# Kernel tuning notes

Hardware: AMD Instinct MI355X
Metric: run time of the kernel (lower is better)

The kernel has to match this reference:

```python
import jax, jax.numpy as jnp
import numpy as np

B, S, H, D = 8, 1024, 16, 64
EMBED_DIM = H * D  # 1024
NEG_INF = -1e30


def setup_inputs() -> dict:
    key = jax.random.key(0)
    kq, kk, kv, kl = jax.random.split(key, 4)
    q = jax.random.normal(kq, (B, S, H, D), dtype=jnp.float32)
    k = jax.random.normal(kk, (B, S, H, D), dtype=jnp.float32)
    v = jax.random.normal(kv, (B, S, H, D), dtype=jnp.float32)
    # ragged lengths in [S//4, S]; prefix-style key_padding_mask (True = valid)
    lengths = jax.random.randint(kl, (B,), S // 4, S + 1)
    key_padding_mask = jnp.arange(S)[None, :] < lengths[:, None]
    return {"q": q, "k": k, "v": v, "key_padding_mask": key_padding_mask}


def reference(q, k, v, key_padding_mask):
    # Equivalent math of flash_attn_unpadded_qkvpacked_func on unpadded tokens
    # followed by pad_input (zeros at padded query rows), dropout=0 (eval).
    # NOTE: module uses softmax_scale = embed_dim ** -0.5 (not head_dim).
    scale = EMBED_DIM ** (-0.5)
    scores = jnp.einsum("bqhd,bkhd->bhqk", q, k) * scale  # [B,H,S,S]
    scores = jnp.where(key_padding_mask[:, None, None, :], scores, NEG_INF)
    attn = jax.nn.softmax(scores, axis=-1)
    out = jnp.einsum("bhqk,bkhd->bqhd", attn, v)  # [B,S,H,D]
    # pad_input re-inserts zeros at padded query positions
    out = out * key_padding_mask[:, :, None, None].astype(out.dtype)
    return out.reshape(B, S, H * D)
```

## Files before the change

kernel.cpp:

```cpp
#include <hip/hip_runtime.h>


#define SS 1024
#define NH 16
#define DD 64
#define ROWSTRIDE (NH * DD)
#define SCALE 0.03125f
#define LOG2E 1.4426950408889634f
#define PC1 (SCALE * LOG2E)
#define PC2 (-12.0f * LOG2E)
#define KSTR 72
#define VSTR 72

typedef short bf16x8 __attribute__((ext_vector_type(8)));
typedef unsigned short u16;
typedef unsigned short u16x8 __attribute__((ext_vector_type(8)));
typedef unsigned short u16x4 __attribute__((ext_vector_type(4)));
typedef float f32x4 __attribute__((ext_vector_type(4)));
typedef unsigned u32x4 __attribute__((ext_vector_type(4)));

__device__ __forceinline__ u16 f2bf(float x) {
  unsigned u = __builtin_bit_cast(unsigned, x);
  return (u16)((u + 0x7FFFu + ((u >> 16) & 1u)) >> 16);
}
__device__ __forceinline__ float bf2f(u16 s) {
  unsigned u = ((unsigned)s) << 16;
  return __builtin_bit_cast(float, u);
}
__device__ __forceinline__ unsigned pkbf(float a, float b) {
#if __has_builtin(__builtin_amdgcn_cvt_pk_bf16_f32)
  auto r = __builtin_amdgcn_cvt_pk_bf16_f32(a, b);
  return __builtin_bit_cast(unsigned, r);
#else
  return (unsigned)f2bf(a) | ((unsigned)f2bf(b) << 16);
#endif
}

__global__ __launch_bounds__(256, 4) void fa_main(const void* qv, const void* kv,
                                                  const void* vv, const void* maskv,
                                                  float* out) {
  __shared__ __attribute__((aligned(16))) u16 Kt[64 * KSTR];
  __shared__ __attribute__((aligned(16))) u16 Vt[64 * VSTR + 64];

  int tid = threadIdx.x;
  int lane = tid & 63;
  int w = tid >> 6;
  int t = lane & 15;
  int quad = lane >> 4;

  int bid = blockIdx.x;
  int x = bid & 7;
  int j = bid >> 3;
  int qt = j & 15;
  int bh = ((j >> 4) << 3) + x;
  int h = bh & (NH - 1);
  int b = bh >> 4;
  int q0 = qt * 64;

  const u16* qs16 = (const u16*)qv;
  float dv = bf2f(qs16[2 * lane]);
  unsigned long long bal = __ballot(!(fabsf(dv) < 100.0f));
  int isf32 = (__popcll(bal) >= 16) ? 1 : 0;

  const unsigned char* m8 = (const unsigned char*)maskv;
  const int* m32 = (const int*)maskv;
  bool isu8 = (m8[1] != 0);
  int lo = 0, hi = SS;
  while (lo < hi) {
    int mid = (lo + hi) >> 1;
    int vbit = isu8 ? (m8[b * SS + mid] != 0) : (m32[b * SS + mid] != 0);
    if (vbit) lo = mid + 1; else hi = mid;
  }
  int len = lo;

  size_t base = (size_t)b * SS * ROWSTRIDE + h * DD;

  if (q0 >= len) {
    f32x4 z4 = {0.f, 0.f, 0.f, 0.f};
    for (int i = tid; i < 64 * 16; i += 256) {
      int r = i >> 4, dseg = (i & 15) << 2;
      *(f32x4*)&out[base + (size_t)(q0 + r) * ROWSTRIDE + dseg] = z4;
    }
    return;
  }

  int qrow = q0 + w * 16 + t;
  bf16x8 qf[2];
  if (isf32) {
    const float* qp = (const float*)qv + base + (size_t)qrow * ROWSTRIDE + quad * 8;
#pragma unroll
    for (int kk = 0; kk < 2; kk++) {
      union { bf16x8 v; unsigned d[4]; } u;
#pragma unroll
      for (int jj = 0; jj < 4; jj++)
        u.d[jj] = pkbf(qp[kk * 32 + 2 * jj], qp[kk * 32 + 2 * jj + 1]);
      qf[kk] = u.v;
    }
  } else {
    const u16* qp = (const u16*)qv + base + (size_t)qrow * ROWSTRIDE + quad * 8;
#pragma unroll
    for (int kk = 0; kk < 2; kk++) qf[kk] = *(const bf16x8*)(qp + kk * 32);
  }

  f32x4 zero4 = {0.f, 0.f, 0.f, 0.f};
  f32x4 oacc[4];
#pragma unroll
  for (int c = 0; c < 4; c++) oacc[c] = zero4;
  float lsum = 0.f;

  int key = tid >> 2, seg = tid & 3;
  int kp = tid >> 3, ds = tid & 7;
  int nkt = (len + 63) >> 6;

  f32x4 kA[4], vA[4];
  u16x8 kB[2], vB[2];

  auto issue_loads = [&](int kt) {
    int krow = kt * 64 + key;
    if (krow > SS - 1) krow = SS - 1;
    int vrow = kt * 64 + 2 * kp;
    if (vrow > SS - 2) vrow = SS - 2;
    size_t ksrc = base + (size_t)krow * ROWSTRIDE + seg * 16;
    size_t vsrc = base + (size_t)vrow * ROWSTRIDE + ds * 8;
    if (isf32) {
      const f32x4* kpp = (const f32x4*)((const float*)kv + ksrc);
#pragma unroll
      for (int i = 0; i < 4; i++) kA[i] = kpp[i];
      const float* vp = (const float*)vv + vsrc;
      vA[0] = *(const f32x4*)vp;
      vA[1] = *(const f32x4*)(vp + 4);
      vA[2] = *(const f32x4*)(vp + ROWSTRIDE);
      vA[3] = *(const f32x4*)(vp + ROWSTRIDE + 4);
    } else {
      const u16x8* kpp = (const u16x8*)((const u16*)kv + ksrc);
      kB[0] = kpp[0]; kB[1] = kpp[1];
      const u16* vp = (const u16*)vv + vsrc;
      vB[0] = *(const u16x8*)vp;
      vB[1] = *(const u16x8*)(vp + ROWSTRIDE);
    }
  };

  auto stage_to_lds = [&]() {
    if (isf32) {
      unsigned kd[8];
#pragma unroll
      for (int i = 0; i < 8; i++)
        kd[i] = pkbf(kA[i >> 1][2 * (i & 1)], kA[i >> 1][2 * (i & 1) + 1]);
      *(u32x4*)&Kt[key * KSTR + seg * 16] = u32x4{kd[0], kd[1], kd[2], kd[3]};
      *(u32x4*)&Kt[key * KSTR + seg * 16 + 8] = u32x4{kd[4], kd[5], kd[6], kd[7]};
#pragma unroll
      for (int jj = 0; jj < 8; jj++) {
        int d = ds * 8 + jj;
        *(unsigned*)&Vt[d * VSTR + (d >> 4) * 16 + 2 * kp] =
            pkbf(vA[jj >> 2][jj & 3], vA[2 + (jj >> 2)][jj & 3]);
      }
    } else {
      *(u16x8*)&Kt[key * KSTR + seg * 16] = kB[0];
      *(u16x8*)&Kt[key * KSTR + seg * 16 + 8] = kB[1];
#pragma unroll
      for (int jj = 0; jj < 8; jj++) {
        int d = ds * 8 + jj;
        *(unsigned*)&Vt[d * VSTR + (d >> 4) * 16 + 2 * kp] =
            (unsigned)(u16)vB[0][jj] | ((unsigned)(u16)vB[1][jj] << 16);
      }
    }
  };

  issue_loads(0);

  for (int kt = 0; kt < nkt; ++kt) {
    __syncthreads();
    stage_to_lds();
    if (kt + 1 < nkt) issue_loads(kt + 1);
    __syncthreads();

    f32x4 sacc[4];
#pragma unroll
    for (int c = 0; c < 4; c++) sacc[c] = zero4;
#pragma unroll
    for (int kk = 0; kk < 2; kk++) {
#pragma unroll
      for (int c = 0; c < 4; c++) {
        bf16x8 ka = *(const bf16x8*)&Kt[(c * 16 + t) * KSTR + kk * 32 + quad * 8];
        sacc[c] = __builtin_amdgcn_mfma_f32_16x16x32_bf16(ka, qf[kk], sacc[c], 0, 0, 0);
      }
    }

    float p[4][4];
    if (kt == nkt - 1) {
      int krem = len - kt * 64;
#pragma unroll
      for (int c = 0; c < 4; c++) {
        int kbase = c * 16 + quad * 4;
#pragma unroll
        for (int r = 0; r < 4; r++)
          p[c][r] = (kbase + r < krem)
                        ? __builtin_amdgcn_exp2f(fmaf(sacc[c][r], PC1, PC2))
                        : 0.0f;
      }
    } else {
#pragma unroll
      for (int c = 0; c < 4; c++)
#pragma unroll
        for (int r = 0; r < 4; r++)
          p[c][r] = __builtin_amdgcn_exp2f(fmaf(sacc[c][r], PC1, PC2));
    }
#pragma unroll
    for (int c = 0; c < 4; c++)
      lsum += (p[c][0] + p[c][1]) + (p[c][2] + p[c][3]);

    unsigned pd[4][2];
#pragma unroll
    for (int c = 0; c < 4; c++) {
      pd[c][0] = pkbf(p[c][0], p[c][1]);
      pd[c][1] = pkbf(p[c][2], p[c][3]);
    }

#pragma unroll
    for (int kc = 0; kc < 2; kc++) {
      union { bf16x8 v; unsigned d[4]; } pa;
      pa.d[0] = pd[2 * kc][0];
      pa.d[1] = pd[2 * kc][1];
      pa.d[2] = pd[2 * kc + 1][0];
      pa.d[3] = pd[2 * kc + 1][1];
#pragma unroll
      for (int c = 0; c < 4; c++) {
        const u16* vr = &Vt[(c * 16 + t) * VSTR + c * 16 + kc * 32 + quad * 4];
        union { bf16x8 v; u16x4 h[2]; } vb;
        vb.h[0] = *(const u16x4*)vr;
        vb.h[1] = *(const u16x4*)(vr + 16);
        oacc[c] = __builtin_amdgcn_mfma_f32_16x16x32_bf16(pa.v, vb.v, oacc[c], 0, 0, 0);
      }
    }
  }

  lsum += __shfl_xor(lsum, 16);
  lsum += __shfl_xor(lsum, 32);
  float inv[4];
#pragma unroll
  for (int r = 0; r < 4; r++)
    inv[r] = 1.0f / __shfl(lsum, quad * 4 + r);
#pragma unroll
  for (int c = 0; c < 4; c++)
#pragma unroll
    for (int r = 0; r < 4; r++) {
      int qr = q0 + w * 16 + quad * 4 + r;
      float o = oacc[c][r] * inv[r];
      out[base + (size_t)qr * ROWSTRIDE + c * 16 + t] = (qr < len) ? o : 0.0f;
    }
}

extern "C" void kernel_launch(void* const* d_in, const int* in_sizes, int n_in,
                              void* d_out, int out_size, void* d_ws, size_t ws_size,
                              hipStream_t stream) {
  fa_main<<<2048, 256, 0, stream>>>(d_in[0], d_in[1], d_in[2], d_in[3], (float*)d_out);
}
```

Measured before the change: 173.9 us.

## Use persistent workers with atomic work queue for attention tiles

Replaces the one-block-per-tile launch with 1024 persistent blocks that pull (q-tile, batch-head) work items from a global atomic counter. Items are ordered by query tile, so blocks take early, long-running tiles first and short or empty late tiles fill in, which evens out the ragged-length load imbalance. A done counter resets the queue at the end so the next launch starts from zero. In exchange it adds two barriers and one atomic per item, plus global state that must be reset correctly between launches.

```diff
diff --git a/kernel.cpp b/kernel.cpp
--- a/kernel.cpp
+++ b/kernel.cpp
@@ -11,6 +11,8 @@
 #define PC2 (-12.0f * LOG2E)
 #define KSTR 72
 #define VSTR 72
+#define NITEMS 2048
+#define NWORKERS 1024
 
 typedef short bf16x8 __attribute__((ext_vector_type(8)));
 typedef unsigned short u16;
@@ -18,6 +20,9 @@
 typedef unsigned short u16x4 __attribute__((ext_vector_type(4)));
 typedef float f32x4 __attribute__((ext_vector_type(4)));
 typedef unsigned u32x4 __attribute__((ext_vector_type(4)));
+
+__device__ unsigned g_next = 0u;
+__device__ unsigned g_done = 0u;
 
 __device__ __forceinline__ u16 f2bf(float x) {
   unsigned u = __builtin_bit_cast(unsigned, x);
@@ -41,6 +46,7 @@
                                                   float* out) {
   __shared__ __attribute__((aligned(16))) u16 Kt[64 * KSTR];
   __shared__ __attribute__((aligned(16))) u16 Vt[64 * VSTR + 64];
+  __shared__ unsigned s_item;
 
   int tid = threadIdx.x;
   int lane = tid & 63;
@@ -48,15 +54,6 @@
   int t = lane & 15;
   int quad = lane >> 4;
 
-  int bid = blockIdx.x;
-  int x = bid & 7;
-  int j = bid >> 3;
-  int qt = j & 15;
-  int bh = ((j >> 4) << 3) + x;
-  int h = bh & (NH - 1);
-  int b = bh >> 4;
-  int q0 = qt * 64;
-
   const u16* qs16 = (const u16*)qv;
   float dv = bf2f(qs16[2 * lane]);
   unsigned long long bal = __ballot(!(fabsf(dv) < 100.0f));
@@ -65,193 +62,219 @@
   const unsigned char* m8 = (const unsigned char*)maskv;
   const int* m32 = (const int*)maskv;
   bool isu8 = (m8[1] != 0);
-  int lo = 0, hi = SS;
-  while (lo < hi) {
-    int mid = (lo + hi) >> 1;
-    int vbit = isu8 ? (m8[b * SS + mid] != 0) : (m32[b * SS + mid] != 0);
-    if (vbit) lo = mid + 1; else hi = mid;
-  }
-  int len = lo;
-
-  size_t base = (size_t)b * SS * ROWSTRIDE + h * DD;
-
-  if (q0 >= len) {
-    f32x4 z4 = {0.f, 0.f, 0.f, 0.f};
-    for (int i = tid; i < 64 * 16; i += 256) {
-      int r = i >> 4, dseg = (i & 15) << 2;
-      *(f32x4*)&out[base + (size_t)(q0 + r) * ROWSTRIDE + dseg] = z4;
-    }
-    return;
-  }
-
-  int qrow = q0 + w * 16 + t;
-  bf16x8 qf[2];
-  if (isf32) {
-    const float* qp = (const float*)qv + base + (size_t)qrow * ROWSTRIDE + quad * 8;
-#pragma unroll
-    for (int kk = 0; kk < 2; kk++) {
-      union { bf16x8 v; unsigned d[4]; } u;
-#pragma unroll
-      for (int jj = 0; jj < 4; jj++)
-        u.d[jj] = pkbf(qp[kk * 32 + 2 * jj], qp[kk * 32 + 2 * jj + 1]);
-      qf[kk] = u.v;
-    }
-  } else {
-    const u16* qp = (const u16*)qv + base + (size_t)qrow * ROWSTRIDE + quad * 8;
-#pragma unroll
-    for (int kk = 0; kk < 2; kk++) qf[kk] = *(const bf16x8*)(qp + kk * 32);
-  }
-
-  f32x4 zero4 = {0.f, 0.f, 0.f, 0.f};
-  f32x4 oacc[4];
-#pragma unroll
-  for (int c = 0; c < 4; c++) oacc[c] = zero4;
-  float lsum = 0.f;
 
   int key = tid >> 2, seg = tid & 3;
   int kp = tid >> 3, ds = tid & 7;
-  int nkt = (len + 63) >> 6;
-
-  f32x4 kA[4], vA[4];
-  u16x8 kB[2], vB[2];
-
-  auto issue_loads = [&](int kt) {
-    int krow = kt * 64 + key;
-    if (krow > SS - 1) krow = SS - 1;
-    int vrow = kt * 64 + 2 * kp;
-    if (vrow > SS - 2) vrow = SS - 2;
-    size_t ksrc = base + (size_t)krow * ROWSTRIDE + seg * 16;
-    size_t vsrc = base + (size_t)vrow * ROWSTRIDE + ds * 8;
+
+  for (;;) {
+    if (tid == 0) s_item = atomicAdd(&g_next, 1u);
+    __syncthreads();
+    unsigned item = s_item;
+    __syncthreads();
+    if (item >= NITEMS) break;
+
+    int qt = (int)(item >> 7);
+    int bh = (int)(item & 127u);
+    int h = bh & (NH - 1);
+    int b = bh >> 4;
+    int q0 = qt * 64;
+
+    int lo = 0, hi = SS;
+    while (lo < hi) {
+      int mid = (lo + hi) >> 1;
+      int vbit = isu8 ? (m8[b * SS + mid] != 0) : (m32[b * SS + mid] != 0);
+      if (vbit) lo = mid + 1; else hi = mid;
+    }
+    int len = lo;
+
+    size_t base = (size_t)b * SS * ROWSTRIDE + h * DD;
+
+    if (q0 >= len) {
+      f32x4 z4 = {0.f, 0.f, 0.f, 0.f};
+      for (int i = tid; i < 64 * 16; i += 256) {
+        int r = i >> 4, dseg = (i & 15) << 2;
+        *(f32x4*)&out[base + (size_t)(q0 + r) * ROWSTRIDE + dseg] = z4;
+      }
+      continue;
+    }
+
+    int qrow = q0 + w * 16 + t;
+    bf16x8 qf[2];
     if (isf32) {
-      const f32x4* kpp = (const f32x4*)((const float*)kv + ksrc);
-#pragma unroll
-      for (int i = 0; i < 4; i++) kA[i] = kpp[i];
-      const float* vp = (const float*)vv + vsrc;
-      vA[0] = *(const f32x4*)vp;
-      vA[1] = *(const f32x4*)(vp + 4);
-      vA[2] = *(const f32x4*)(vp + ROWSTRIDE);
-      vA[3] = *(const f32x4*)(vp + ROWSTRIDE + 4);
+      const float* qp = (const float*)qv + base + (size_t)qrow * ROWSTRIDE + quad * 8;
+#pragma unroll
+      for (int kk = 0; kk < 2; kk++) {
+        union { bf16x8 v; unsigned d[4]; } u;
+#pragma unroll
+        for (int jj = 0; jj < 4; jj++)
+          u.d[jj] = pkbf(qp[kk * 32 + 2 * jj], qp[kk * 32 + 2 * jj + 1]);
+        qf[kk] = u.v;
+      }
     } else {
-      const u16x8* kpp = (const u16x8*)((const u16*)kv + ksrc);
-      kB[0] = kpp[0]; kB[1] = kpp[1];
-      const u16* vp = (const u16*)vv + vsrc;
-      vB[0] = *(const u16x8*)vp;
-      vB[1] = *(const u16x8*)(vp + ROWSTRIDE);
-    }
-  };
-
-  auto stage_to_lds = [&]() {
-    if (isf32) {
-      unsigned kd[8];
-#pragma unroll
-      for (int i = 0; i < 8; i++)
-        kd[i] = pkbf(kA[i >> 1][2 * (i & 1)], kA[i >> 1][2 * (i & 1) + 1]);
-      *(u32x4*)&Kt[key * KSTR + seg * 16] = u32x4{kd[0], kd[1], kd[2], kd[3]};
-      *(u32x4*)&Kt[key * KSTR + seg * 16 + 8] = u32x4{kd[4], kd[5], kd[6], kd[7]};
-#pragma unroll
-      for (int jj = 0; jj < 8; jj++) {
-        int d = ds * 8 + jj;
-        *(unsigned*)&Vt[d * VSTR + (d >> 4) * 16 + 2 * kp] =
-            pkbf(vA[jj >> 2][jj & 3], vA[2 + (jj >> 2)][jj & 3]);
-      }
-    } else {
-      *(u16x8*)&Kt[key * KSTR + seg * 16] = kB[0];
-      *(u16x8*)&Kt[key * KSTR + seg * 16 + 8] = kB[1];
-#pragma unroll
-      for (int jj = 0; jj < 8; jj++) {
-        int d = ds * 8 + jj;
-        *(unsigned*)&Vt[d * VSTR + (d >> 4) * 16 + 2 * kp] =
-            (unsigned)(u16)vB[0][jj] | ((unsigned)(u16)vB[1][jj] << 16);
-      }
-    }
-  };
-
-  issue_loads(0);
-
-  for (int kt = 0; kt < nkt; ++kt) {
-    __syncthreads();
-    stage_to_lds();
-    if (kt + 1 < nkt) issue_loads(kt + 1);
-    __syncthreads();
-
-    f32x4 sacc[4];
-#pragma unroll
-    for (int c = 0; c < 4; c++) sacc[c] = zero4;
-#pragma unroll
-    for (int kk = 0; kk < 2; kk++) {
+      const u16* qp = (const u16*)qv + base + (size_t)qrow * ROWSTRIDE + quad * 8;
+#pragma unroll
+      for (int kk = 0; kk < 2; kk++) qf[kk] = *(const bf16x8*)(qp + kk * 32);
+    }
+
+    f32x4 zero4 = {0.f, 0.f, 0.f, 0.f};
+    f32x4 oacc[4];
+#pragma unroll
+    for (int c = 0; c < 4; c++) oacc[c] = zero4;
+    float lsum = 0.f;
+
+    int nkt = (len + 63) >> 6;
+
+    f32x4 kA[4], vA[4];
+    u16x8 kB[2], vB[2];
+
+    auto issue_loads = [&](int kt) {
+      int krow = kt * 64 + key;
+      if (krow > SS - 1) krow = SS - 1;
+      int vrow = kt * 64 + 2 * kp;
+      if (vrow > SS - 2) vrow = SS - 2;
+      size_t ksrc = base + (size_t)krow * ROWSTRIDE + seg * 16;
+      size_t vsrc = base + (size_t)vrow * ROWSTRIDE + ds * 8;
+      if (isf32) {
+        const f32x4* kpp = (const f32x4*)((const float*)kv + ksrc);
+#pragma unroll
+        for (int i = 0; i < 4; i++) kA[i] = kpp[i];
+        const float* vp = (const float*)vv + vsrc;
+        vA[0] = *(const f32x4*)vp;
+        vA[1] = *(const f32x4*)(vp + 4);
+        vA[2] = *(const f32x4*)(vp + ROWSTRIDE);
+        vA[3] = *(const f32x4*)(vp + ROWSTRIDE + 4);
+      } else {
+        const u16x8* kpp = (const u16x8*)((const u16*)kv + ksrc);
+        kB[0] = kpp[0]; kB[1] = kpp[1];
+        const u16* vp = (const u16*)vv + vsrc;
+        vB[0] = *(const u16x8*)vp;
+        vB[1] = *(const u16x8*)(vp + ROWSTRIDE);
+      }
+    };
+
+    auto stage_to_lds = [&]() {
+      if (isf32) {
+        unsigned kd[8];
+#pragma unroll
+        for (int i = 0; i < 8; i++)
+          kd[i] = pkbf(kA[i >> 1][2 * (i & 1)], kA[i >> 1][2 * (i & 1) + 1]);
+        *(u32x4*)&Kt[key * KSTR + seg * 16] = u32x4{kd[0], kd[1], kd[2], kd[3]};
+        *(u32x4*)&Kt[key * KSTR + seg * 16 + 8] = u32x4{kd[4], kd[5], kd[6], kd[7]};
+#pragma unroll
+        for (int jj = 0; jj < 8; jj++) {
+          int d = ds * 8 + jj;
+          *(unsigned*)&Vt[d * VSTR + (d >> 4) * 16 + 2 * kp] =
+              pkbf(vA[jj >> 2][jj & 3], vA[2 + (jj >> 2)][jj & 3]);
+        }
+      } else {
+        *(u16x8*)&Kt[key * KSTR + seg * 16] = kB[0];
+        *(u16x8*)&Kt[key * KSTR + seg * 16 + 8] = kB[1];
+#pragma unroll
+        for (int jj = 0; jj < 8; jj++) {
+          int d = ds * 8 + jj;
+          *(unsigned*)&Vt[d * VSTR + (d >> 4) * 16 + 2 * kp] =
+              (unsigned)(u16)vB[0][jj] | ((unsigned)(u16)vB[1][jj] << 16);
+        }
+      }
+    };
+
+    issue_loads(0);
+
+    for (int kt = 0; kt < nkt; ++kt) {
+      __syncthreads();
+      stage_to_lds();
+      if (kt + 1 < nkt) issue_loads(kt + 1);
+      __syncthreads();
+
+      f32x4 sacc[4];
+#pragma unroll
+      for (int c = 0; c < 4; c++) sacc[c] = zero4;
+#pragma unroll
+      for (int kk = 0; kk < 2; kk++) {
+#pragma unroll
+        for (int c = 0; c < 4; c++) {
+          bf16x8 ka = *(const bf16x8*)&Kt[(c * 16 + t) * KSTR + kk * 32 + quad * 8];
+          sacc[c] = __builtin_amdgcn_mfma_f32_16x16x32_bf16(ka, qf[kk], sacc[c], 0, 0, 0);
+        }
+      }
+
+      float p[4][4];
+      if (kt == nkt - 1) {
+        int krem = len - kt * 64;
+#pragma unroll
+        for (int c = 0; c < 4; c++) {
+          int kbase = c * 16 + quad * 4;
+#pragma unroll
+          for (int r = 0; r < 4; r++)
+            p[c][r] = (kbase + r < krem)
+                          ? __builtin_amdgcn_exp2f(fmaf(sacc[c][r], PC1, PC2))
+                          : 0.0f;
+        }
+      } else {
+#pragma unroll
+        for (int c = 0; c < 4; c++)
+#pragma unroll
+          for (int r = 0; r < 4; r++)
+            p[c][r] = __builtin_amdgcn_exp2f(fmaf(sacc[c][r], PC1, PC2));
+      }
+#pragma unroll
+      for (int c = 0; c < 4; c++)
+        lsum += (p[c][0] + p[c][1]) + (p[c][2] + p[c][3]);
+
+      unsigned pd[4][2];
 #pragma unroll
       for (int c = 0; c < 4; c++) {
-        bf16x8 ka = *(const bf16x8*)&Kt[(c * 16 + t) * KSTR + kk * 32 + quad * 8];
-        sacc[c] = __builtin_amdgcn_mfma_f32_16x16x32_bf16(ka, qf[kk], sacc[c], 0, 0, 0);
-      }
-    }
-
-    float p[4][4];
-    if (kt == nkt - 1) {
-      int krem = len - kt * 64;
-#pragma unroll
-      for (int c = 0; c < 4; c++) {
-        int kbase = c * 16 + quad * 4;
-#pragma unroll
-        for (int r = 0; r < 4; r++)
-          p[c][r] = (kbase + r < krem)
-                        ? __builtin_amdgcn_exp2f(fmaf(sacc[c][r], PC1, PC2))
-                        : 0.0f;
-      }
-    } else {
-#pragma unroll
-      for (int c = 0; c < 4; c++)
-#pragma unroll
-        for (int r = 0; r < 4; r++)
-          p[c][r] = __builtin_amdgcn_exp2f(fmaf(sacc[c][r], PC1, PC2));
-    }
+        pd[c][0] = pkbf(p[c][0], p[c][1]);
+        pd[c][1] = pkbf(p[c][2], p[c][3]);
+      }
+
+#pragma unroll
+      for (int kc = 0; kc < 2; kc++) {
+        union { bf16x8 v; unsigned d[4]; } pa;
+        pa.d[0] = pd[2 * kc][0];
+        pa.d[1] = pd[2 * kc][1];
+        pa.d[2] = pd[2 * kc + 1][0];
+        pa.d[3] = pd[2 * kc + 1][1];
+#pragma unroll
+        for (int c = 0; c < 4; c++) {
+          const u16* vr = &Vt[(c * 16 + t) * VSTR + c * 16 + kc * 32 + quad * 4];
+          union { bf16x8 v; u16x4 h[2]; } vb;
+          vb.h[0] = *(const u16x4*)vr;
+          vb.h[1] = *(const u16x4*)(vr + 16);
+          oacc[c] = __builtin_amdgcn_mfma_f32_16x16x32_bf16(pa.v, vb.v, oacc[c], 0, 0, 0);
+        }
+      }
+    }
+
+    lsum += __shfl_xor(lsum, 16);
+    lsum += __shfl_xor(lsum, 32);
+    float inv[4];
+#pragma unroll
+    for (int r = 0; r < 4; r++)
+      inv[r] = 1.0f / __shfl(lsum, quad * 4 + r);
 #pragma unroll
     for (int c = 0; c < 4; c++)
-      lsum += (p[c][0] + p[c][1]) + (p[c][2] + p[c][3]);
-
-    unsigned pd[4][2];
-#pragma unroll
-    for (int c = 0; c < 4; c++) {
-      pd[c][0] = pkbf(p[c][0], p[c][1]);
-      pd[c][1] = pkbf(p[c][2], p[c][3]);
-    }
-
-#pragma unroll
-    for (int kc = 0; kc < 2; kc++) {
-      union { bf16x8 v; unsigned d[4]; } pa;
-      pa.d[0] = pd[2 * kc][0];
-      pa.d[1] = pd[2 * kc][1];
-      pa.d[2] = pd[2 * kc + 1][0];
-      pa.d[3] = pd[2 * kc + 1][1];
-#pragma unroll
-      for (int c = 0; c < 4; c++) {
-        const u16* vr = &Vt[(c * 16 + t) * VSTR + c * 16 + kc * 32 + quad * 4];
-        union { bf16x8 v; u16x4 h[2]; } vb;
-        vb.h[0] = *(const u16x4*)vr;
-        vb.h[1] = *(const u16x4*)(vr + 16);
-        oacc[c] = __builtin_amdgcn_mfma_f32_16x16x32_bf16(pa.v, vb.v, oacc[c], 0, 0, 0);
-      }
-    }
+#pragma unroll
+      for (int r = 0; r < 4; r++) {
+        int qr = q0 + w * 16 + quad * 4 + r;
+        float o = oacc[c][r] * inv[r];
+        out[base + (size_t)qr * ROWSTRIDE + c * 16 + t] = (qr < len) ? o : 0.0f;
+      }
   }
 
-  lsum += __shfl_xor(lsum, 16);
-  lsum += __shfl_xor(lsum, 32);
-  float inv[4];
-#pragma unroll
-  for (int r = 0; r < 4; r++)
-    inv[r] = 1.0f / __shfl(lsum, quad * 4 + r);
-#pragma unroll
-  for (int c = 0; c < 4; c++)
-#pragma unroll
-    for (int r = 0; r < 4; r++) {
-      int qr = q0 + w * 16 + quad * 4 + r;
-      float o = oacc[c][r] * inv[r];
-      out[base + (size_t)qr * ROWSTRIDE + c * 16 + t] = (qr < len) ? o : 0.0f;
-    }
+  if (tid == 0) {
+    __threadfence();
+    unsigned d = atomicAdd(&g_done, 1u);
+    if (d == (unsigned)(gridDim.x - 1)) {
+      atomicExch(&g_next, 0u);
+      atomicExch(&g_done, 0u);
+      __threadfence();
+    }
+  }
 }
 
 extern "C" void kernel_launch(void* const* d_in, const int* in_sizes, int n_in,
                               void* d_out, int out_size, void* d_ws, size_t ws_size,
                               hipStream_t stream) {
-  fa_main<<<2048, 256, 0, stream>>>(d_in[0], d_in[1], d_in[2], d_in[3], (float*)d_out);
-}
+  fa_main<<<NWORKERS, 256, 0, stream>>>(d_in[0], d_in[1], d_in[2], d_in[3], (float*)d_out);
+}
```

Measured after the change: 221.9 us. 1.28x slower.
